# Performance work log

Measured on AMD Instinct MI355X. Metric: run time of the kernel, lower is better.

The kernel has to match this reference:

```python
import jax, jax.numpy as jnp
import numpy as np

B, S, D_IN, D_E = 8, 2048, 1024, 1024


def setup_inputs() -> dict:
    key = jax.random.key(0)
    ks = jax.random.split(key, 9)
    s_in = 1.0 / np.sqrt(D_IN)
    s_e = 1.0 / np.sqrt(D_E)
    return {
        "x": jax.random.normal(ks[0], (B, S, D_IN), dtype=jnp.float32),
        "Wq": jax.random.uniform(ks[1], (D_IN, D_E), jnp.float32, -s_in, s_in),
        "bq": jax.random.uniform(ks[2], (D_E,), jnp.float32, -s_in, s_in),
        "Wk": jax.random.uniform(ks[3], (D_IN, D_E), jnp.float32, -s_in, s_in),
        "bk": jax.random.uniform(ks[4], (D_E,), jnp.float32, -s_in, s_in),
        "Wv": jax.random.uniform(ks[5], (D_IN, D_E), jnp.float32, -s_in, s_in),
        "bv": jax.random.uniform(ks[6], (D_E,), jnp.float32, -s_in, s_in),
        "Wo": jax.random.uniform(ks[7], (D_E, D_E), jnp.float32, -s_e, s_e),
        "bo": jax.random.uniform(ks[8], (D_E,), jnp.float32, -s_e, s_e),
    }


def reference(x, Wq, bq, Wk, bk, Wv, bv, Wo, bo):
    # QKV projections: [B,S,D_in] @ [D_in,D_e] -> [B,S,D_e]
    Q = jnp.einsum("bsi,ie->bse", x, Wq) + bq
    K = jnp.einsum("bsi,ie->bse", x, Wk) + bk
    V = jnp.einsum("bsi,ie->bse", x, Wv) + bv
    scale = 1.0 / jnp.sqrt(jnp.asarray(Q.shape[-1], Q.dtype))
    # full score matrix [B,S,S] (faithful to the unfused original)
    logits = jnp.einsum("bqe,bke->bqk", Q, K) * scale
    attn = jax.nn.softmax(logits, axis=-1)
    values = jnp.einsum("bqk,bke->bqe", attn, V)
    o = jnp.einsum("bqe,ef->bqf", values, Wo) + bo
    return o
```

## Files before the change

### kernel.cpp

```cpp
#include <hip/hip_runtime.h>

#define DIN 1024
#define DE  1024
#define SEQ 2048
#define NB  8

typedef __bf16 bf16x8 __attribute__((ext_vector_type(8)));
typedef float  f32x4  __attribute__((ext_vector_type(4)));
typedef unsigned short u16;
typedef u16 u16x8 __attribute__((ext_vector_type(8)));
typedef u16 u16x4 __attribute__((ext_vector_type(4)));

__device__ __forceinline__ u16 f2bf(float f) {
  unsigned u = __builtin_bit_cast(unsigned, f);
  return (u16)((u + 0x7FFFu + ((u >> 16) & 1u)) >> 16);
}
__device__ __forceinline__ float bf2f(u16 h) {
  return __builtin_bit_cast(float, (unsigned)h << 16);
}

typedef __attribute__((address_space(1))) const unsigned char g_u8;
typedef __attribute__((address_space(3))) unsigned char l_u8;
__device__ __forceinline__ void gload16(const void* g, void* l) {
  __builtin_amdgcn_global_load_lds((g_u8*)g, (l_u8*)l, 16, 0, 0);
}

__global__ __launch_bounds__(256) void cvt_f32_bf16(const float* __restrict__ in,
                                                    u16* __restrict__ out, int n4) {
  int i = blockIdx.x * 256 + threadIdx.x;
  if (i >= n4) return;
  float4 v = ((const float4*)in)[i];
  u16x4 o;
  o[0] = f2bf(v.x); o[1] = f2bf(v.y); o[2] = f2bf(v.z); o[3] = f2bf(v.w);
  ((u16x4*)out)[i] = o;
}

__global__ __launch_bounds__(256) void transpose_w(const float* __restrict__ W,
                                                   u16* __restrict__ Wt) {
  __shared__ float t[32][33];
  const int tx = threadIdx.x, ty = threadIdx.y;
  const int bx = blockIdx.x * 32, by = blockIdx.y * 32;
#pragma unroll
  for (int i = 0; i < 4; ++i)
    t[ty + i * 8][tx] = W[(size_t)(by + ty + i * 8) * 1024 + bx + tx];
  __syncthreads();
#pragma unroll
  for (int i = 0; i < 4; ++i)
    Wt[(size_t)(bx + ty + i * 8) * 1024 + by + tx] = f2bf(t[tx][ty + i * 8]);
}

__global__ __launch_bounds__(256) void softmax_rows_bf16(u16* __restrict__ P) {
  const size_t row = blockIdx.x;
  u16* pr = P + row * 2048 + (size_t)threadIdx.x * 8;
  u16x8 v = *(const u16x8*)pr;
  float x[8];
#pragma unroll
  for (int j = 0; j < 8; ++j) x[j] = bf2f(v[j]);
  float m = x[0];
#pragma unroll
  for (int j = 1; j < 8; ++j) m = fmaxf(m, x[j]);
#pragma unroll
  for (int off = 32; off; off >>= 1) m = fmaxf(m, __shfl_xor(m, off));
  __shared__ float rm[4], rs[4];
  const int lane = threadIdx.x & 63, wid = threadIdx.x >> 6;
  if (lane == 0) rm[wid] = m;
  __syncthreads();
  m = fmaxf(fmaxf(rm[0], rm[1]), fmaxf(rm[2], rm[3]));
  float s = 0.f;
#pragma unroll
  for (int j = 0; j < 8; ++j) { x[j] = __expf(x[j] - m); s += x[j]; }
#pragma unroll
  for (int off = 32; off; off >>= 1) s += __shfl_xor(s, off);
  if (lane == 0) rs[wid] = s;
  __syncthreads();
  s = (rs[0] + rs[1]) + (rs[2] + rs[3]);
  const float inv = 1.f / s;
  u16x8 o;
#pragma unroll
  for (int j = 0; j < 8; ++j) o[j] = f2bf(x[j] * inv);
  *(u16x8*)pr = o;
}

template <int OMODE, bool HAS_BIAS>
__global__ __launch_bounds__(512) void gemm3b(
    const u16* __restrict__ A, const u16* __restrict__ Bt, void* __restrict__ Cv,
    const float* __restrict__ bias, int M, int N, int K,
    size_t sA, size_t sB, size_t sC, float scale) {
  constexpr int BUF = 32768;
  __shared__ __align__(16) char lds[3 * BUF];
  const int tid = threadIdx.x, lane = tid & 63, wid = tid >> 6;
  const int wm = wid >> 2, wn = wid & 3;
  const int lane15 = lane & 15, gk = lane >> 4;

  const int gx = gridDim.x, gy = gridDim.y;
  int lin = blockIdx.x + gx * (blockIdx.y + gy * blockIdx.z);
  const int nwg = gx * gy * (int)gridDim.z;
  const int q = nwg >> 3, r8 = nwg & 7;
  const int xcd = lin & 7, idx = lin >> 3;
  lin = (xcd < r8 ? xcd * (q + 1) : r8 * (q + 1) + (xcd - r8) * q) + idx;
  const int bz = lin / (gx * gy);
  const int rem = lin - bz * (gx * gy);
  const int by = rem / gx, bx = rem - (rem / gx) * gx;

  const char* Ag = (const char*)(A + (size_t)bz * sA + (size_t)by * 256 * K);
  const char* Bg = (const char*)(Bt + (size_t)bz * sB + (size_t)bx * 256 * K);
  const size_t Kb = (size_t)K * 2;

  const char* sa[2];
  const char* sb[2];
  int dA[2], dB[2];
#pragma unroll
  for (int j = 0; j < 2; ++j) {
    const int ls = j * 512 + tid, pr = ls >> 2, ps = ls & 3;
    const int g = ps ^ ((pr >> 1) & 3);
    sa[j] = Ag + (size_t)pr * Kb + g * 16;
    sb[j] = Bg + (size_t)pr * Kb + g * 16;
    dA[j] = ls * 16;
    dB[j] = 16384 + ls * 16;
  }

  int aoff[8], boff[4];
#pragma unroll
  for (int m = 0; m < 8; ++m) {
    const int r = wm * 128 + m * 16 + lane15;
    aoff[m] = r * 64 + ((gk ^ ((r >> 1) & 3)) << 4);
  }
#pragma unroll
  for (int n = 0; n < 4; ++n) {
    const int r = wn * 64 + n * 16 + lane15;
    boff[n] = 16384 + r * 64 + ((gk ^ ((r >> 1) & 3)) << 4);
  }

  f32x4 acc[8][4] = {};
  const int NT = K >> 5;

  auto stage = [&](int b) {
    char* base = lds + b * BUF;
#pragma unroll
    for (int j = 0; j < 2; ++j) {
      gload16(sa[j], base + dA[j]);
      gload16(sb[j], base + dB[j]);
      sa[j] += 64; sb[j] += 64;
    }
  };

  stage(0); stage(1);
  asm volatile("s_waitcnt vmcnt(4)" ::: "memory");
  __builtin_amdgcn_s_barrier();
  __builtin_amdgcn_sched_barrier(0);

  int cur = 0;
  for (int t = 0; t < NT; ++t) {
    if (t + 2 < NT) stage(cur == 0 ? 2 : cur - 1);
    const char* base = lds + cur * BUF;
    bf16x8 af[8], bfv[4];
#pragma unroll
    for (int n = 0; n < 4; ++n) bfv[n] = *(const bf16x8*)(base + boff[n]);
#pragma unroll
    for (int m = 0; m < 8; ++m) af[m] = *(const bf16x8*)(base + aoff[m]);
    __builtin_amdgcn_s_setprio(1);
#pragma unroll
    for (int m = 0; m < 8; ++m)
#pragma unroll
      for (int n = 0; n < 4; ++n)
        acc[m][n] = __builtin_amdgcn_mfma_f32_16x16x32_bf16(af[m], bfv[n], acc[m][n], 0, 0, 0);
    __builtin_amdgcn_s_setprio(0);
    if (t < NT - 2)       asm volatile("s_waitcnt vmcnt(4)" ::: "memory");
    else if (t == NT - 2) asm volatile("s_waitcnt vmcnt(0)" ::: "memory");
    __builtin_amdgcn_s_barrier();
    __builtin_amdgcn_sched_barrier(0);
    cur = cur == 2 ? 0 : cur + 1;
  }

  const int rbase = by * 256 + wm * 128 + (gk << 2);
  const int cbase = bx * 256 + wn * 64 + lane15;
#pragma unroll
  for (int m = 0; m < 8; ++m)
#pragma unroll
    for (int n = 0; n < 4; ++n) {
      const int col = cbase + n * 16;
      const float bval = HAS_BIAS ? bias[col] : 0.f;
#pragma unroll
      for (int r = 0; r < 4; ++r) {
        const int rowg = rbase + m * 16 + r;
        const float v = acc[m][n][r] * scale + bval;
        if (OMODE == 0)
          ((float*)Cv)[(size_t)bz * sC + (size_t)rowg * N + col] = v;
        else if (OMODE == 1)
          ((u16*)Cv)[(size_t)bz * sC + (size_t)rowg * N + col] = f2bf(v);
        else
          ((u16*)Cv)[(size_t)(rowg >> 11) * ((size_t)DE * SEQ) +
                     (size_t)col * SEQ + (rowg & 2047)] = f2bf(v);
      }
    }
}

extern "C" void kernel_launch(void* const* d_in, const int* in_sizes, int n_in,
                              void* d_out, int out_size, void* d_ws, size_t ws_size,
                              hipStream_t stream) {
  const float* x  = (const float*)d_in[0];
  const float* Wq = (const float*)d_in[1];
  const float* bq = (const float*)d_in[2];
  const float* Wk = (const float*)d_in[3];
  const float* bk = (const float*)d_in[4];
  const float* Wv = (const float*)d_in[5];
  const float* bv = (const float*)d_in[6];
  const float* Wo = (const float*)d_in[7];
  const float* bo = (const float*)d_in[8];

  const size_t NEED = 142606336;
  if (ws_size < NEED) return;
  char* ws = (char*)d_ws;
  u16* x_bf = (u16*)(ws);
  u16* q_bf = (u16*)(ws + 33554432);
  u16* k_bf = (u16*)(ws + 67108864);
  u16* vt   = (u16*)(ws + 100663296);
  u16* wt   = (u16*)(ws + 134217728);
  u16* lgP  = (u16*)d_out;
  u16* wt_q = wt;
  u16* wt_k = wt + 1048576;
  u16* wt_v = wt + 2097152;
  u16* wt_o = wt + 3145728;

  dim3 tb(32, 8);
  const size_t sQ = (size_t)SEQ * DE;
  const size_t sL = (size_t)SEQ * SEQ;

  cvt_f32_bf16<<<16384, 256, 0, stream>>>(x, x_bf, (NB * SEQ * DIN) / 4);
  transpose_w<<<dim3(32, 32), tb, 0, stream>>>(Wq, wt_q);
  transpose_w<<<dim3(32, 32), tb, 0, stream>>>(Wk, wt_k);
  transpose_w<<<dim3(32, 32), tb, 0, stream>>>(Wv, wt_v);
  transpose_w<<<dim3(32, 32), tb, 0, stream>>>(Wo, wt_o);
  gemm3b<1, true><<<dim3(4, 64, 1), 512, 0, stream>>>(x_bf, wt_q, q_bf, bq,
      16384, 1024, 1024, 0, 0, 0, 1.f);
  gemm3b<1, true><<<dim3(4, 64, 1), 512, 0, stream>>>(x_bf, wt_k, k_bf, bk,
      16384, 1024, 1024, 0, 0, 0, 1.f);
  gemm3b<2, true><<<dim3(4, 64, 1), 512, 0, stream>>>(x_bf, wt_v, vt, bv,
      16384, 1024, 1024, 0, 0, 0, 1.f);
  gemm3b<1, false><<<dim3(8, 8, 8), 512, 0, stream>>>(q_bf, k_bf, lgP,
      nullptr, 2048, 2048, 1024, sQ, sQ, sL, 0.03125f);
  softmax_rows_bf16<<<16384, 256, 0, stream>>>(lgP);
  gemm3b<1, false><<<dim3(4, 8, 8), 512, 0, stream>>>(lgP, vt, q_bf,
      nullptr, 2048, 1024, 2048, sL, sQ, sQ, 1.f);
  gemm3b<0, true><<<dim3(4, 64, 1), 512, 0, stream>>>(q_bf, wt_o, d_out, bo,
      16384, 1024, 1024, 0, 0, 0, 1.f);

  (void)in_sizes; (void)n_in; (void)out_size; (void)ws_size;
}
```

Measured before the change: 345.4 us.

## Fuse QKV projections into one GEMM and double-buffer LDS fragment reads

Merges the three Q/K/V projection GEMMs into a single launch over the concatenated transposed weights. The epilogue routes each column range to its own output, bias and layout. The GEMM mainloop moves from a 3-stage to a 4-stage LDS ring and adds register ping-pong, so the LDS fragment reads for the next k-step overlap the MFMAs of the current one. The extra register sets and 128KB LDS with launch_bounds(512,2) raise register and occupancy pressure, so performance could suffer if the compiler spills.

Result: slower. 388.4 us (+12.4%).

```diff
diff --git a/kernel.cpp b/kernel.cpp
--- a/kernel.cpp
+++ b/kernel.cpp
@@ -81,13 +81,31 @@
   *(u16x8*)pr = o;
 }
 
+#define READF(BUFI, AV, BV)                                                   \
+  {                                                                           \
+    const char* _b = lds + (BUFI) * 32768;                                    \
+    _Pragma("unroll") for (int n_ = 0; n_ < 4; ++n_)                          \
+        BV[n_] = *(const bf16x8*)(_b + boffB + n_ * 1024);                    \
+    _Pragma("unroll") for (int m_ = 0; m_ < 8; ++m_)                          \
+        AV[m_] = *(const bf16x8*)(_b + aoffB + m_ * 1024);                    \
+  }
+#define MFMAF(AV, BV)                                                         \
+  {                                                                           \
+    __builtin_amdgcn_s_setprio(1);                                            \
+    _Pragma("unroll") for (int m_ = 0; m_ < 8; ++m_)                          \
+        _Pragma("unroll") for (int n_ = 0; n_ < 4; ++n_)                      \
+            acc[m_][n_] = __builtin_amdgcn_mfma_f32_16x16x32_bf16(            \
+                AV[m_], BV[n_], acc[m_][n_], 0, 0, 0);                        \
+    __builtin_amdgcn_s_setprio(0);                                            \
+  }
+
 template <int OMODE, bool HAS_BIAS>
-__global__ __launch_bounds__(512) void gemm3b(
-    const u16* __restrict__ A, const u16* __restrict__ Bt, void* __restrict__ Cv,
-    const float* __restrict__ bias, int M, int N, int K,
-    size_t sA, size_t sB, size_t sC, float scale) {
-  constexpr int BUF = 32768;
-  __shared__ __align__(16) char lds[3 * BUF];
+__global__ __launch_bounds__(512, 2) void gemmrp(
+    const u16* __restrict__ A, const u16* __restrict__ Bt, void* __restrict__ C0,
+    u16* __restrict__ C1, u16* __restrict__ C2, const float* __restrict__ b0,
+    const float* __restrict__ b1, const float* __restrict__ b2,
+    int M, int Nout, int K, size_t sA, size_t sB, size_t sC, float scale) {
+  __shared__ __align__(16) char lds[4 * 32768];
   const int tid = threadIdx.x, lane = tid & 63, wid = tid >> 6;
   const int wm = wid >> 2, wn = wid & 3;
   const int lane15 = lane & 15, gk = lane >> 4;
@@ -118,24 +136,8 @@
     dA[j] = ls * 16;
     dB[j] = 16384 + ls * 16;
   }
-
-  int aoff[8], boff[4];
-#pragma unroll
-  for (int m = 0; m < 8; ++m) {
-    const int r = wm * 128 + m * 16 + lane15;
-    aoff[m] = r * 64 + ((gk ^ ((r >> 1) & 3)) << 4);
-  }
-#pragma unroll
-  for (int n = 0; n < 4; ++n) {
-    const int r = wn * 64 + n * 16 + lane15;
-    boff[n] = 16384 + r * 64 + ((gk ^ ((r >> 1) & 3)) << 4);
-  }
-
-  f32x4 acc[8][4] = {};
-  const int NT = K >> 5;
-
   auto stage = [&](int b) {
-    char* base = lds + b * BUF;
+    char* base = lds + b * 32768;
 #pragma unroll
     for (int j = 0; j < 2; ++j) {
       gload16(sa[j], base + dA[j]);
@@ -144,32 +146,37 @@
     }
   };
 
-  stage(0); stage(1);
+  const int sw = (gk ^ ((lane15 >> 1) & 3)) << 4;
+  const int aoffB = wm * 8192 + lane15 * 64 + sw;
+  const int boffB = 16384 + wn * 4096 + lane15 * 64 + sw;
+
+  f32x4 acc[8][4] = {};
+  bf16x8 pa[8], pb[4], qa[8], qb[4];
+  const int NT = K >> 5;
+
+  stage(0); stage(1); stage(2);
   asm volatile("s_waitcnt vmcnt(4)" ::: "memory");
   __builtin_amdgcn_s_barrier();
   __builtin_amdgcn_sched_barrier(0);
-
-  int cur = 0;
-  for (int t = 0; t < NT; ++t) {
-    if (t + 2 < NT) stage(cur == 0 ? 2 : cur - 1);
-    const char* base = lds + cur * BUF;
-    bf16x8 af[8], bfv[4];
-#pragma unroll
-    for (int n = 0; n < 4; ++n) bfv[n] = *(const bf16x8*)(base + boff[n]);
-#pragma unroll
-    for (int m = 0; m < 8; ++m) af[m] = *(const bf16x8*)(base + aoff[m]);
-    __builtin_amdgcn_s_setprio(1);
-#pragma unroll
-    for (int m = 0; m < 8; ++m)
-#pragma unroll
-      for (int n = 0; n < 4; ++n)
-        acc[m][n] = __builtin_amdgcn_mfma_f32_16x16x32_bf16(af[m], bfv[n], acc[m][n], 0, 0, 0);
-    __builtin_amdgcn_s_setprio(0);
-    if (t < NT - 2)       asm volatile("s_waitcnt vmcnt(4)" ::: "memory");
-    else if (t == NT - 2) asm volatile("s_waitcnt vmcnt(0)" ::: "memory");
+  READF(0, pa, pb);
+
+  for (int t = 0; t < NT; t += 2) {
+    if (t + 3 < NT) stage((t + 3) & 3);
+    READF((t + 1) & 3, qa, qb);
+    __builtin_amdgcn_sched_barrier(0);
+    MFMAF(pa, pb);
+    if (t + 3 < NT) asm volatile("s_waitcnt vmcnt(4)" ::: "memory");
+    else            asm volatile("s_waitcnt vmcnt(0)" ::: "memory");
     __builtin_amdgcn_s_barrier();
     __builtin_amdgcn_sched_barrier(0);
-    cur = cur == 2 ? 0 : cur + 1;
+    if (t + 4 < NT) stage((t + 4) & 3);
+    if (t + 2 < NT) READF((t + 2) & 3, pa, pb);
+    __builtin_amdgcn_sched_barrier(0);
+    MFMAF(qa, qb);
+    if (t + 4 < NT) asm volatile("s_waitcnt vmcnt(4)" ::: "memory");
+    else            asm volatile("s_waitcnt vmcnt(0)" ::: "memory");
+    __builtin_amdgcn_s_barrier();
+    __builtin_amdgcn_sched_barrier(0);
   }
 
   const int rbase = by * 256 + wm * 128 + (gk << 2);
@@ -179,18 +186,33 @@
 #pragma unroll
     for (int n = 0; n < 4; ++n) {
       const int col = cbase + n * 16;
-      const float bval = HAS_BIAS ? bias[col] : 0.f;
-#pragma unroll
-      for (int r = 0; r < 4; ++r) {
-        const int rowg = rbase + m * 16 + r;
-        const float v = acc[m][n][r] * scale + bval;
-        if (OMODE == 0)
-          ((float*)Cv)[(size_t)bz * sC + (size_t)rowg * N + col] = v;
-        else if (OMODE == 1)
-          ((u16*)Cv)[(size_t)bz * sC + (size_t)rowg * N + col] = f2bf(v);
-        else
-          ((u16*)Cv)[(size_t)(rowg >> 11) * ((size_t)DE * SEQ) +
-                     (size_t)col * SEQ + (rowg & 2047)] = f2bf(v);
+      if (OMODE == 3) {
+        u16* Cp; int ccol; const float* bp;
+        if (col < 1024)      { Cp = (u16*)C0; ccol = col;        bp = b0; }
+        else if (col < 2048) { Cp = C1;       ccol = col - 1024; bp = b1; }
+        else                 { Cp = C2;       ccol = col - 2048; bp = b2; }
+        const float bval = bp[ccol];
+#pragma unroll
+        for (int r = 0; r < 4; ++r) {
+          const int rowg = rbase + m * 16 + r;
+          const float v = acc[m][n][r] + bval;
+          if (col < 2048)
+            Cp[(size_t)rowg * 1024 + ccol] = f2bf(v);
+          else
+            Cp[(size_t)(rowg >> 11) * ((size_t)DE * SEQ) +
+               (size_t)ccol * SEQ + (rowg & 2047)] = f2bf(v);
+        }
+      } else {
+        const float bval = HAS_BIAS ? b0[col] : 0.f;
+#pragma unroll
+        for (int r = 0; r < 4; ++r) {
+          const int rowg = rbase + m * 16 + r;
+          const float v = acc[m][n][r] * scale + bval;
+          if (OMODE == 0)
+            ((float*)C0)[(size_t)bz * sC + (size_t)rowg * Nout + col] = v;
+          else
+            ((u16*)C0)[(size_t)bz * sC + (size_t)rowg * Nout + col] = f2bf(v);
+        }
       }
     }
 }
@@ -231,19 +253,18 @@
   transpose_w<<<dim3(32, 32), tb, 0, stream>>>(Wk, wt_k);
   transpose_w<<<dim3(32, 32), tb, 0, stream>>>(Wv, wt_v);
   transpose_w<<<dim3(32, 32), tb, 0, stream>>>(Wo, wt_o);
-  gemm3b<1, true><<<dim3(4, 64, 1), 512, 0, stream>>>(x_bf, wt_q, q_bf, bq,
+  gemmrp<3, true><<<dim3(12, 64, 1), 512, 0, stream>>>(x_bf, wt, q_bf, k_bf, vt,
+      bq, bk, bv, 16384, 1024, 1024, 0, 0, 0, 1.f);
+  gemmrp<1, false><<<dim3(8, 8, 8), 512, 0, stream>>>(q_bf, k_bf, lgP,
+      nullptr, nullptr, nullptr, nullptr, nullptr,
+      2048, 2048, 1024, sQ, sQ, sL, 0.03125f);
+  softmax_rows_bf16<<<16384, 256, 0, stream>>>(lgP);
+  gemmrp<1, false><<<dim3(4, 8, 8), 512, 0, stream>>>(lgP, vt, q_bf,
+      nullptr, nullptr, nullptr, nullptr, nullptr,
+      2048, 1024, 2048, sL, sQ, sQ, 1.f);
+  gemmrp<0, true><<<dim3(4, 64, 1), 512, 0, stream>>>(q_bf, wt_o, d_out,
+      nullptr, nullptr, bo, nullptr, nullptr,
       16384, 1024, 1024, 0, 0, 0, 1.f);
-  gemm3b<1, true><<<dim3(4, 64, 1), 512, 0, stream>>>(x_bf, wt_k, k_bf, bk,
-      16384, 1024, 1024, 0, 0, 0, 1.f);
-  gemm3b<2, true><<<dim3(4, 64, 1), 512, 0, stream>>>(x_bf, wt_v, vt, bv,
-      16384, 1024, 1024, 0, 0, 0, 1.f);
-  gemm3b<1, false><<<dim3(8, 8, 8), 512, 0, stream>>>(q_bf, k_bf, lgP,
-      nullptr, 2048, 2048, 1024, sQ, sQ, sL, 0.03125f);
-  softmax_rows_bf16<<<16384, 256, 0, stream>>>(lgP);
-  gemm3b<1, false><<<dim3(4, 8, 8), 512, 0, stream>>>(lgP, vt, q_bf,
-      nullptr, 2048, 1024, 2048, sL, sQ, sQ, 1.f);
-  gemm3b<0, true><<<dim3(4, 64, 1), 512, 0, stream>>>(q_bf, wt_o, d_out, bo,
-      16384, 1024, 1024, 0, 0, 0, 1.f);
 
   (void)in_sizes; (void)n_in; (void)out_size; (void)ws_size;
 }
```
